# Kernel optimization log

Hardware: AMD Instinct MI355X
Metric: run time of the kernel (lower is better)

## Reference

```python
import jax, jax.numpy as jnp
import numpy as np
from jax import lax

K = 3      # kernel_size
PAD = 1    # padding (stride=1, dilation=1, groups=1 as in torchvision defaults)


def setup_inputs() -> dict:
    key = jax.random.key(0)
    ks = jax.random.split(key, 4)
    B, C, O, H, W = 4, 256, 256, 64, 64
    x = jax.random.normal(ks[0], (B, C, H, W), jnp.float32)
    # offset-predictor conv weights: small scale so predicted offsets are a few pixels
    w_off = jax.random.normal(ks[1], (2 * K * K, C, K, K), jnp.float32) * 0.01
    b_off = jnp.zeros((2 * K * K,), jnp.float32)
    # main deformable conv weights (kaiming-ish scale)
    w_def = jax.random.normal(ks[2], (O, C, K, K), jnp.float32) * (1.0 / np.sqrt(C * K * K))
    b_def = jnp.zeros((O,), jnp.float32)
    return {"x": x, "w_off": w_off, "b_off": b_off, "w_def": w_def, "b_def": b_def}


def _deform_conv(x, w_off, b_off, w_def, b_def):
    B, C, H, W = x.shape
    O = w_def.shape[0]
    KK = K * K
    # 1) predict offsets with a standard conv: [B, 2*K*K, H, W]
    offsets = lax.conv_general_dilated(x, w_off, (1, 1), [(PAD, PAD), (PAD, PAD)])
    offsets = offsets + b_off[None, :, None, None]
    # torchvision layout: channel 2*k is dy, 2*k+1 is dx for kernel tap k = ky*K+kx
    off = offsets.reshape(B, KK, 2, H, W)
    ky, kx = jnp.meshgrid(jnp.arange(K, dtype=jnp.float32),
                          jnp.arange(K, dtype=jnp.float32), indexing='ij')
    # sampling coords py/px: [B, KK, H, W]
    py = off[:, :, 0] + (jnp.arange(H, dtype=jnp.float32)[None, None, :, None]
                         + ky.reshape(-1)[None, :, None, None] - PAD)
    px = off[:, :, 1] + (jnp.arange(W, dtype=jnp.float32)[None, None, None, :]
                         + kx.reshape(-1)[None, :, None, None] - PAD)
    y0 = jnp.floor(py)
    x0 = jnp.floor(px)
    ly = py - y0
    lx = px - x0
    x_flat = x.reshape(B, C, H * W)
    gather = jax.vmap(lambda xf, ix: xf[:, ix])  # per-batch gather over spatial index
    sampled = jnp.zeros((B, C, KK, H, W), x.dtype)
    # bilinear interpolation with zero padding outside the image (4 corners)
    for dy_, wy in ((0.0, 1.0 - ly), (1.0, ly)):
        yi = y0 + dy_
        for dx_, wx in ((0.0, 1.0 - lx), (1.0, lx)):
            xi = x0 + dx_
            valid = (yi >= 0) & (yi < H) & (xi >= 0) & (xi < W)
            yc = jnp.clip(yi, 0, H - 1).astype(jnp.int32)
            xc = jnp.clip(xi, 0, W - 1).astype(jnp.int32)
            idx = (yc * W + xc).reshape(B, -1)               # [B, KK*H*W]
            vals = gather(x_flat, idx).reshape(B, C, KK, H, W)
            wgt = (wy * wx * valid).astype(x.dtype)          # [B, KK, H, W]
            sampled = sampled + vals * wgt[:, None]
    # 3) contract sampled patches with the deform-conv weight
    out = jnp.einsum('bckhw,ock->bohw', sampled, w_def.reshape(O, C, KK))
    return out + b_def[None, :, None, None]


def reference(x, w_off, b_off, w_def, b_def):
    return _deform_conv(x, w_off, b_off, w_def, b_def)
```

## Files before the change

kernel.cpp:

```cpp
#include <hip/hip_runtime.h>

#define B_ 4
#define C_ 256
#define O_ 256
#define H_ 64
#define W_ 64
#define HW 4096
#define NOFF 18
#define CK 2304

typedef __bf16 bf16x8 __attribute__((ext_vector_type(8)));
typedef float f32x4 __attribute__((ext_vector_type(4)));

__global__ __launch_bounds__(256) void wprep_def_kernel(
    const float* __restrict__ w_def, uint4* __restrict__ Wt4)
{
    const int gidx = blockIdx.x * 256 + threadIdx.x;
    const int ch = gidx >> 11;
    const int rem = gidx & 2047;
    const int o = rem >> 3, g = rem & 7;
    const int kk = ch >> 2, cg = ch & 3;
    bf16x8 v;
#pragma unroll
    for (int j = 0; j < 8; ++j) {
        const int c = cg * 64 + g * 8 + j;
        v[j] = (__bf16)w_def[(size_t)o * CK + c * 9 + kk];
    }
    Wt4[(size_t)ch * 2048 + o * 8 + (g ^ (o & 7))] = __builtin_bit_cast(uint4, v);
}

__global__ __launch_bounds__(256) void wprep_woff_kernel(
    const float* __restrict__ w_off, uint4* __restrict__ Woff4)
{
    const int ch = blockIdx.x;
    const int t = threadIdx.x;
    const int o = t >> 3, g = t & 7;
    const int kk = ch >> 2, cg = ch & 3;
    bf16x8 v;
#pragma unroll
    for (int j = 0; j < 8; ++j) {
        const int c = cg * 64 + g * 8 + j;
        v[j] = (o < NOFF) ? (__bf16)w_off[(size_t)o * CK + c * 9 + kk] : (__bf16)0.f;
    }
    Woff4[(size_t)ch * 256 + o * 8 + (g ^ (o & 7))] = __builtin_bit_cast(uint4, v);
}

__global__ __launch_bounds__(512, 1) void deform_fused_kernel(
    const float* __restrict__ x, const uint4* __restrict__ Wt4,
    const uint4* __restrict__ Woff4, const float* __restrict__ b_off,
    const float* __restrict__ b_def, float* __restrict__ out)
{
    __shared__ uint4 slab[4096];
    __shared__ uint4 Wl4[2048];
    __shared__ uint4 Sl4[512];
    __shared__ uint4 woff_lds[256];
    __shared__ float offs_lds[NOFF * 64];

    const int i = blockIdx.x;
    const int l = ((i & 7) << 5) + (i >> 3);
    const int b = l >> 6, h = l & 63;
    const int wb = h - 3;

    const int t = threadIdx.x;
    const int lane = t & 63;
    const int w = t >> 6;
    const int l15 = lane & 15, l4 = lane >> 4;
    const int sp = t & 63;
    const int sg = w;
    const float* xb = x + (size_t)b * C_ * HW;

    auto stage_slab = [&](int cg) {
        const float* xc = xb + (size_t)(cg * 64 + sg * 8) * HW;
#pragma unroll
        for (int r = 0; r < 8; ++r) {
            const int yc = min(max(wb + r, 0), H_ - 1);
            bf16x8 v;
#pragma unroll
            for (int j = 0; j < 8; ++j)
                v[j] = (__bf16)xc[(size_t)j * HW + yc * W_ + sp];
            slab[(r * 64 + sp) * 8 + (sg ^ (sp & 7))] = __builtin_bit_cast(uint4, v);
        }
    };

    f32x4 acc_off0 = {0.f, 0.f, 0.f, 0.f}, acc_off1 = {0.f, 0.f, 0.f, 0.f};
    for (int cg = 0; cg < 4; ++cg) {
        stage_slab(cg);
        __syncthreads();
        for (int kk = 0; kk < 9; ++kk) {
            if (t < 256) woff_lds[t] = Woff4[(size_t)(kk * 4 + cg) * 256 + t];
            const int ky = kk / 3, kx = kk - 3 * ky;
            const int y = h + ky - 1;
            const int col = sp + kx - 1;
            uint4 sv = {0u, 0u, 0u, 0u};
            if (y >= 0 && y < H_ && col >= 0 && col < W_)
                sv = slab[((ky + 2) * 64 + col) * 8 + (sg ^ (col & 7))];
            Sl4[sp * 8 + (sg ^ (sp & 7))] = sv;
            __syncthreads();
            if (w < 4) {
#pragma unroll
                for (int st = 0; st < 2; ++st) {
                    const int g = st * 4 + l4;
                    const int pr = w * 16 + l15;
                    const bf16x8 bF = __builtin_bit_cast(bf16x8, Sl4[pr * 8 + (g ^ (pr & 7))]);
                    const int r0 = l15, r1 = 16 + l15;
                    const bf16x8 a0 = __builtin_bit_cast(bf16x8, woff_lds[r0 * 8 + (g ^ (r0 & 7))]);
                    const bf16x8 a1 = __builtin_bit_cast(bf16x8, woff_lds[r1 * 8 + (g ^ (r1 & 7))]);
                    acc_off0 = __builtin_amdgcn_mfma_f32_16x16x32_bf16(a0, bF, acc_off0, 0, 0, 0);
                    acc_off1 = __builtin_amdgcn_mfma_f32_16x16x32_bf16(a1, bF, acc_off1, 0, 0, 0);
                }
            }
            __syncthreads();
        }
    }
    if (w < 4) {
#pragma unroll
        for (int ii = 0; ii < 2; ++ii) {
            const f32x4 a = ii ? acc_off1 : acc_off0;
#pragma unroll
            for (int r = 0; r < 4; ++r) {
                const int oc = ii * 16 + l4 * 4 + r;
                if (oc < NOFF)
                    offs_lds[oc * 64 + (w * 16 + l15)] = a[r] + b_off[oc];
            }
        }
    }
    __syncthreads();

    const int wo = w >> 1, wp = w & 1;
    f32x4 acc[4][2];
#pragma unroll
    for (int ii = 0; ii < 4; ++ii)
#pragma unroll
        for (int j = 0; j < 2; ++j) acc[ii][j] = f32x4{0.f, 0.f, 0.f, 0.f};

    for (int cgi = 0; cgi < 4; ++cgi) {
        const int cg = 3 - cgi;
        if (cgi != 0) {
            stage_slab(cg);
            __syncthreads();
        }
        const float* xsg = xb + (size_t)(cg * 64 + sg * 8) * HW;
        for (int kk = 0; kk < 9; ++kk) {
            const uint4* wsrc = Wt4 + (size_t)(kk * 4 + cg) * 2048;
#pragma unroll
            for (int r = 0; r < 4; ++r)
                Wl4[t + 512 * r] = wsrc[t + 512 * r];
            const int ky = kk / 3, kx = kk - 3 * ky;
            const float dy = offs_lds[(2 * kk) * 64 + sp];
            const float dx = offs_lds[(2 * kk + 1) * 64 + sp];
            const float py = (float)(h + ky - 1) + dy;
            const float pxf = (float)(sp + kx - 1) + dx;
            const float y0f = floorf(py), x0f = floorf(pxf);
            const float ly = py - y0f, lx = pxf - x0f;
            const int y0 = (int)y0f, x0 = (int)x0f;
            const int y1 = y0 + 1, x1 = x0 + 1;
            const bool vy0 = (y0 >= 0) && (y0 < H_), vy1 = (y1 >= 0) && (y1 < H_);
            const bool vx0 = (x0 >= 0) && (x0 < W_), vx1 = (x1 >= 0) && (x1 < W_);
            const float w00 = (vy0 && vx0) ? (1.f - ly) * (1.f - lx) : 0.f;
            const float w01 = (vy0 && vx1) ? (1.f - ly) * lx : 0.f;
            const float w10 = (vy1 && vx0) ? ly * (1.f - lx) : 0.f;
            const float w11 = (vy1 && vx1) ? ly * lx : 0.f;
            bf16x8 sv;
            if (y0 >= wb && y0 <= wb + 6) {
                const int s0 = y0 - wb;
                const int xc0 = min(max(x0, 0), W_ - 1);
                const int xc1 = min(max(x1, 0), W_ - 1);
                const int gx0 = sg ^ (xc0 & 7), gx1 = sg ^ (xc1 & 7);
                const bf16x8 c00 = __builtin_bit_cast(bf16x8, slab[(s0 * 64 + xc0) * 8 + gx0]);
                const bf16x8 c01 = __builtin_bit_cast(bf16x8, slab[(s0 * 64 + xc1) * 8 + gx1]);
                const bf16x8 c10 = __builtin_bit_cast(bf16x8, slab[((s0 + 1) * 64 + xc0) * 8 + gx0]);
                const bf16x8 c11 = __builtin_bit_cast(bf16x8, slab[((s0 + 1) * 64 + xc1) * 8 + gx1]);
#pragma unroll
                for (int j = 0; j < 8; ++j) {
                    const float v = w00 * (float)c00[j] + w01 * (float)c01[j]
                                  + w10 * (float)c10[j] + w11 * (float)c11[j];
                    sv[j] = (__bf16)v;
                }
            } else {
                const int y0c = min(max(y0, 0), H_ - 1), y1c = min(max(y1, 0), H_ - 1);
                const int xc0 = min(max(x0, 0), W_ - 1), xc1 = min(max(x1, 0), W_ - 1);
                const int i00 = y0c * W_ + xc0, i01 = y0c * W_ + xc1;
                const int i10 = y1c * W_ + xc0, i11 = y1c * W_ + xc1;
#pragma unroll
                for (int j = 0; j < 8; ++j) {
                    const float* p = xsg + (size_t)j * HW;
                    const float v = w00 * p[i00] + w01 * p[i01]
                                  + w10 * p[i10] + w11 * p[i11];
                    sv[j] = (__bf16)v;
                }
            }
            Sl4[sp * 8 + (sg ^ (sp & 7))] = __builtin_bit_cast(uint4, sv);
            __syncthreads();
#pragma unroll
            for (int st = 0; st < 2; ++st) {
                const int g = st * 4 + l4;
                bf16x8 aF[4], bF[2];
#pragma unroll
                for (int ii = 0; ii < 4; ++ii) {
                    const int row = wo * 64 + ii * 16 + l15;
                    aF[ii] = __builtin_bit_cast(bf16x8, Wl4[row * 8 + (g ^ (row & 7))]);
                }
#pragma unroll
                for (int j = 0; j < 2; ++j) {
                    const int pr = wp * 32 + j * 16 + l15;
                    bF[j] = __builtin_bit_cast(bf16x8, Sl4[pr * 8 + (g ^ (pr & 7))]);
                }
#pragma unroll
                for (int ii = 0; ii < 4; ++ii)
#pragma unroll
                    for (int j = 0; j < 2; ++j)
                        acc[ii][j] = __builtin_amdgcn_mfma_f32_16x16x32_bf16(
                            aF[ii], bF[j], acc[ii][j], 0, 0, 0);
            }
            __syncthreads();
        }
    }

#pragma unroll
    for (int ii = 0; ii < 4; ++ii) {
#pragma unroll
        for (int r = 0; r < 4; ++r) {
            const int o = wo * 64 + ii * 16 + l4 * 4 + r;
            const float bias = b_def[o];
#pragma unroll
            for (int j = 0; j < 2; ++j) {
                const int p = wp * 32 + j * 16 + l15;
                out[(((size_t)(b * O_ + o)) * H_ + h) * W_ + p] = acc[ii][j][r] + bias;
            }
        }
    }
}

extern "C" void kernel_launch(void* const* d_in, const int* in_sizes, int n_in,
                              void* d_out, int out_size, void* d_ws, size_t ws_size,
                              hipStream_t stream) {
    const float* x     = (const float*)d_in[0];
    const float* w_off = (const float*)d_in[1];
    const float* b_off = (const float*)d_in[2];
    const float* w_def = (const float*)d_in[3];
    const float* b_def = (const float*)d_in[4];
    float* out = (float*)d_out;

    uint4* Wt4   = (uint4*)d_ws;
    uint4* Woff4 = Wt4 + 73728;

    wprep_def_kernel<<<288, 256, 0, stream>>>(w_def, Wt4);
    wprep_woff_kernel<<<36, 256, 0, stream>>>(w_off, Woff4);
    deform_fused_kernel<<<256, 512, 0, stream>>>(x, Wt4, Woff4, b_off, b_def, out);
}
```

Baseline: 156.5 us.

## Split offset conv into separate kernel and halve output channels per block

Moves the offset-predicting conv out of the fused kernel into its own MFMA kernel that reads x straight from global memory and reduces over two channel halves, storing offsets to workspace. The main deformable kernel now covers half the output channels per block, launching twice as many blocks with higher occupancy bounds. It loads weight fragments directly from global into registers instead of staging them in LDS. The weight prep kernel is also changed to transpose each output row through shared memory. The intent is to fill more CUs and drop the serial offset phase and weight LDS traffic, at the cost of recomputing bilinear samples for each output half and an extra kernel launch with a global round-trip for offsets.

```diff
diff --git a/kernel.cpp b/kernel.cpp
--- a/kernel.cpp
+++ b/kernel.cpp
@@ -15,18 +15,22 @@
 __global__ __launch_bounds__(256) void wprep_def_kernel(
     const float* __restrict__ w_def, uint4* __restrict__ Wt4)
 {
-    const int gidx = blockIdx.x * 256 + threadIdx.x;
-    const int ch = gidx >> 11;
-    const int rem = gidx & 2047;
-    const int o = rem >> 3, g = rem & 7;
-    const int kk = ch >> 2, cg = ch & 3;
-    bf16x8 v;
-#pragma unroll
-    for (int j = 0; j < 8; ++j) {
-        const int c = cg * 64 + g * 8 + j;
-        v[j] = (__bf16)w_def[(size_t)o * CK + c * 9 + kk];
-    }
-    Wt4[(size_t)ch * 2048 + o * 8 + (g ^ (o & 7))] = __builtin_bit_cast(uint4, v);
+    __shared__ __bf16 wrow[CK];
+    const int o = blockIdx.x;
+    const int t = threadIdx.x;
+#pragma unroll
+    for (int q = 0; q < 9; ++q)
+        wrow[t * 9 + q] = (__bf16)w_def[(size_t)o * CK + t * 9 + q];
+    __syncthreads();
+    for (int s = t; s < 288; s += 256) {
+        const int ch = s >> 3, g = s & 7;
+        const int kk = ch >> 2, cg = ch & 3;
+        bf16x8 v;
+#pragma unroll
+        for (int j = 0; j < 8; ++j)
+            v[j] = wrow[(cg * 64 + g * 8 + j) * 9 + kk];
+        Wt4[(size_t)ch * 2048 + o * 8 + (g ^ (o & 7))] = __builtin_bit_cast(uint4, v);
+    }
 }
 
 __global__ __launch_bounds__(256) void wprep_woff_kernel(
@@ -45,25 +49,105 @@
     Woff4[(size_t)ch * 256 + o * 8 + (g ^ (o & 7))] = __builtin_bit_cast(uint4, v);
 }
 
-__global__ __launch_bounds__(512, 1) void deform_fused_kernel(
-    const float* __restrict__ x, const uint4* __restrict__ Wt4,
-    const uint4* __restrict__ Woff4, const float* __restrict__ b_off,
-    const float* __restrict__ b_def, float* __restrict__ out)
+__global__ __launch_bounds__(256, 4) void offs_mfma_kernel(
+    const float* __restrict__ x, const uint4* __restrict__ Woff4,
+    const float* __restrict__ b_off, float* __restrict__ offs)
+{
+    __shared__ float red[2][32][16];
+
+    const int i = blockIdx.x;
+    const int l = ((i & 7) << 6) + (i >> 3);
+    const int ph = l & 1;
+    const int bh = l >> 1;
+    const int b = bh >> 6, h = bh & 63;
+
+    const int t = threadIdx.x;
+    const int w = t >> 6, lane = t & 63;
+    const int l15 = lane & 15, l4 = lane >> 4;
+    const int pxg = w & 1, kh = w >> 1;
+    const int px = ph * 32 + pxg * 16 + l15;
+    const float* xb = x + (size_t)b * C_ * HW;
+
+    f32x4 acc0 = {0.f, 0.f, 0.f, 0.f}, acc1 = {0.f, 0.f, 0.f, 0.f};
+
+    for (int kk = 0; kk < 9; ++kk) {
+        const int ky = kk / 3, kx = kk - 3 * ky;
+        const int y = h + ky - 1;
+        const int col = px + kx - 1;
+        const bool valid = (y >= 0) && (y < H_) && (col >= 0) && (col < W_);
+#pragma unroll
+        for (int cgl = 0; cgl < 2; ++cgl) {
+            const int cg = kh * 2 + cgl;
+            const int ch = kk * 4 + cg;
+#pragma unroll
+            for (int st = 0; st < 2; ++st) {
+                const int g = st * 4 + l4;
+                const int r0 = l15, r1 = 16 + l15;
+                const bf16x8 a0 = __builtin_bit_cast(bf16x8,
+                    Woff4[(size_t)ch * 256 + r0 * 8 + (g ^ (r0 & 7))]);
+                const bf16x8 a1 = __builtin_bit_cast(bf16x8,
+                    Woff4[(size_t)ch * 256 + r1 * 8 + (g ^ (r1 & 7))]);
+                bf16x8 bF;
+                if (valid) {
+                    const float* p = xb + (size_t)(cg * 64 + g * 8) * HW + y * W_ + col;
+#pragma unroll
+                    for (int j = 0; j < 8; ++j)
+                        bF[j] = (__bf16)p[(size_t)j * HW];
+                } else {
+#pragma unroll
+                    for (int j = 0; j < 8; ++j) bF[j] = (__bf16)0.f;
+                }
+                acc0 = __builtin_amdgcn_mfma_f32_16x16x32_bf16(a0, bF, acc0, 0, 0, 0);
+                acc1 = __builtin_amdgcn_mfma_f32_16x16x32_bf16(a1, bF, acc1, 0, 0, 0);
+            }
+        }
+    }
+
+    if (kh == 1) {
+#pragma unroll
+        for (int r = 0; r < 4; ++r) {
+            red[pxg][l4 * 4 + r][l15] = acc0[r];
+            red[pxg][16 + l4 * 4 + r][l15] = acc1[r];
+        }
+    }
+    __syncthreads();
+    if (kh == 0) {
+#pragma unroll
+        for (int ii = 0; ii < 2; ++ii) {
+            const f32x4 a = ii ? acc1 : acc0;
+#pragma unroll
+            for (int r = 0; r < 4; ++r) {
+                const int oc = ii * 16 + l4 * 4 + r;
+                if (oc < NOFF) {
+                    const float v = a[r] + red[pxg][oc][l15] + b_off[oc];
+                    offs[((size_t)(bh * 64) + px) * NOFF + oc] = v;
+                }
+            }
+        }
+    }
+}
+
+__global__ __launch_bounds__(512, 4) void deform_mfma_kernel(
+    const float* __restrict__ x, const float* __restrict__ offs,
+    const uint4* __restrict__ Wt4, const float* __restrict__ b_def,
+    float* __restrict__ out)
 {
     __shared__ uint4 slab[4096];
-    __shared__ uint4 Wl4[2048];
     __shared__ uint4 Sl4[512];
-    __shared__ uint4 woff_lds[256];
     __shared__ float offs_lds[NOFF * 64];
 
     const int i = blockIdx.x;
-    const int l = ((i & 7) << 5) + (i >> 3);
-    const int b = l >> 6, h = l & 63;
+    const int l = ((i & 7) << 6) + (i >> 3);
+    const int oh = l & 1;
+    const int bh = l >> 1;
+    const int b = bh >> 6, h = bh & 63;
+    const int obase = oh * 128;
     const int wb = h - 3;
 
     const int t = threadIdx.x;
     const int lane = t & 63;
     const int w = t >> 6;
+    const int wo = w >> 1, wp = w & 1;
     const int l15 = lane & 15, l4 = lane >> 4;
     const int sp = t & 63;
     const int sg = w;
@@ -82,69 +166,34 @@
         }
     };
 
-    f32x4 acc_off0 = {0.f, 0.f, 0.f, 0.f}, acc_off1 = {0.f, 0.f, 0.f, 0.f};
+    for (int idx = t; idx < NOFF * 64; idx += 512) {
+        const int px = idx & 63, oc = idx >> 6;
+        offs_lds[oc * 64 + px] = offs[((size_t)(bh * 64) + px) * NOFF + oc];
+    }
+    stage_slab(0);
+
+    f32x4 acc[2][2];
+#pragma unroll
+    for (int ii = 0; ii < 2; ++ii)
+#pragma unroll
+        for (int j = 0; j < 2; ++j) acc[ii][j] = f32x4{0.f, 0.f, 0.f, 0.f};
+
     for (int cg = 0; cg < 4; ++cg) {
-        stage_slab(cg);
+        if (cg != 0) stage_slab(cg);
         __syncthreads();
-        for (int kk = 0; kk < 9; ++kk) {
-            if (t < 256) woff_lds[t] = Woff4[(size_t)(kk * 4 + cg) * 256 + t];
-            const int ky = kk / 3, kx = kk - 3 * ky;
-            const int y = h + ky - 1;
-            const int col = sp + kx - 1;
-            uint4 sv = {0u, 0u, 0u, 0u};
-            if (y >= 0 && y < H_ && col >= 0 && col < W_)
-                sv = slab[((ky + 2) * 64 + col) * 8 + (sg ^ (col & 7))];
-            Sl4[sp * 8 + (sg ^ (sp & 7))] = sv;
-            __syncthreads();
-            if (w < 4) {
-#pragma unroll
-                for (int st = 0; st < 2; ++st) {
-                    const int g = st * 4 + l4;
-                    const int pr = w * 16 + l15;
-                    const bf16x8 bF = __builtin_bit_cast(bf16x8, Sl4[pr * 8 + (g ^ (pr & 7))]);
-                    const int r0 = l15, r1 = 16 + l15;
-                    const bf16x8 a0 = __builtin_bit_cast(bf16x8, woff_lds[r0 * 8 + (g ^ (r0 & 7))]);
-                    const bf16x8 a1 = __builtin_bit_cast(bf16x8, woff_lds[r1 * 8 + (g ^ (r1 & 7))]);
-                    acc_off0 = __builtin_amdgcn_mfma_f32_16x16x32_bf16(a0, bF, acc_off0, 0, 0, 0);
-                    acc_off1 = __builtin_amdgcn_mfma_f32_16x16x32_bf16(a1, bF, acc_off1, 0, 0, 0);
-                }
-            }
-            __syncthreads();
-        }
-    }
-    if (w < 4) {
-#pragma unroll
-        for (int ii = 0; ii < 2; ++ii) {
-            const f32x4 a = ii ? acc_off1 : acc_off0;
-#pragma unroll
-            for (int r = 0; r < 4; ++r) {
-                const int oc = ii * 16 + l4 * 4 + r;
-                if (oc < NOFF)
-                    offs_lds[oc * 64 + (w * 16 + l15)] = a[r] + b_off[oc];
-            }
-        }
-    }
-    __syncthreads();
-
-    const int wo = w >> 1, wp = w & 1;
-    f32x4 acc[4][2];
-#pragma unroll
-    for (int ii = 0; ii < 4; ++ii)
-#pragma unroll
-        for (int j = 0; j < 2; ++j) acc[ii][j] = f32x4{0.f, 0.f, 0.f, 0.f};
-
-    for (int cgi = 0; cgi < 4; ++cgi) {
-        const int cg = 3 - cgi;
-        if (cgi != 0) {
-            stage_slab(cg);
-            __syncthreads();
-        }
         const float* xsg = xb + (size_t)(cg * 64 + sg * 8) * HW;
         for (int kk = 0; kk < 9; ++kk) {
-            const uint4* wsrc = Wt4 + (size_t)(kk * 4 + cg) * 2048;
-#pragma unroll
-            for (int r = 0; r < 4; ++r)
-                Wl4[t + 512 * r] = wsrc[t + 512 * r];
+            const int ch = kk * 4 + cg;
+            uint4 aR[2][2];
+#pragma unroll
+            for (int st = 0; st < 2; ++st) {
+                const int g = st * 4 + l4;
+#pragma unroll
+                for (int ii = 0; ii < 2; ++ii) {
+                    const int row = obase + wo * 32 + ii * 16 + l15;
+                    aR[st][ii] = Wt4[(size_t)ch * 2048 + row * 8 + (g ^ (row & 7))];
+                }
+            }
             const int ky = kk / 3, kx = kk - 3 * ky;
             const float dy = offs_lds[(2 * kk) * 64 + sp];
             const float dx = offs_lds[(2 * kk + 1) * 64 + sp];
@@ -189,38 +238,35 @@
                     sv[j] = (__bf16)v;
                 }
             }
+            __syncthreads();
             Sl4[sp * 8 + (sg ^ (sp & 7))] = __builtin_bit_cast(uint4, sv);
             __syncthreads();
 #pragma unroll
             for (int st = 0; st < 2; ++st) {
                 const int g = st * 4 + l4;
-                bf16x8 aF[4], bF[2];
-#pragma unroll
-                for (int ii = 0; ii < 4; ++ii) {
-                    const int row = wo * 64 + ii * 16 + l15;
-                    aF[ii] = __builtin_bit_cast(bf16x8, Wl4[row * 8 + (g ^ (row & 7))]);
-                }
+                bf16x8 bF[2];
 #pragma unroll
                 for (int j = 0; j < 2; ++j) {
                     const int pr = wp * 32 + j * 16 + l15;
                     bF[j] = __builtin_bit_cast(bf16x8, Sl4[pr * 8 + (g ^ (pr & 7))]);
                 }
 #pragma unroll
-                for (int ii = 0; ii < 4; ++ii)
+                for (int ii = 0; ii < 2; ++ii)
 #pragma unroll
                     for (int j = 0; j < 2; ++j)
                         acc[ii][j] = __builtin_amdgcn_mfma_f32_16x16x32_bf16(
-                            aF[ii], bF[j], acc[ii][j], 0, 0, 0);
-            }
-            __syncthreads();
-        }
-    }
-
-#pragma unroll
-    for (int ii = 0; ii < 4; ++ii) {
+                            __builtin_bit_cast(bf16x8, aR[st][ii]), bF[j],
+                            acc[ii][j], 0, 0, 0);
+            }
+        }
+        __syncthreads();
+    }
+
+#pragma unroll
+    for (int ii = 0; ii < 2; ++ii) {
 #pragma unroll
         for (int r = 0; r < 4; ++r) {
-            const int o = wo * 64 + ii * 16 + l4 * 4 + r;
+            const int o = obase + wo * 32 + ii * 16 + l4 * 4 + r;
             const float bias = b_def[o];
 #pragma unroll
             for (int j = 0; j < 2; ++j) {
@@ -243,8 +289,10 @@
 
     uint4* Wt4   = (uint4*)d_ws;
     uint4* Woff4 = Wt4 + 73728;
-
-    wprep_def_kernel<<<288, 256, 0, stream>>>(w_def, Wt4);
+    float* offs  = (float*)(Woff4 + 9216);
+
+    wprep_def_kernel<<<256, 256, 0, stream>>>(w_def, Wt4);
     wprep_woff_kernel<<<36, 256, 0, stream>>>(w_off, Woff4);
-    deform_fused_kernel<<<256, 512, 0, stream>>>(x, Wt4, Woff4, b_off, b_def, out);
-}
+    offs_mfma_kernel<<<512, 256, 0, stream>>>(x, Woff4, b_off, offs);
+    deform_mfma_kernel<<<512, 512, 0, stream>>>(x, offs, Wt4, b_def, out);
+}
```

New measurement: 149.5 us. -4.5%, faster.
